# Kernel optimization log

Measured on AMD Instinct MI355X. Metric: run time of the kernel, lower is better.

## Reference

```python
import jax, jax.numpy as jnp
import numpy as np

T, B, I, H = 512, 64, 512, 1024


def setup_inputs() -> dict:
    key = jax.random.key(0)
    ks = jax.random.split(key, 7)
    s = 0.03  # keep recurrent dynamics stable
    return {
        "X": jax.random.normal(ks[0], (T, B, I), jnp.float32),
        "h0": jax.random.normal(ks[1], (B, H), jnp.float32) * 0.1,
        "c0": jax.random.normal(ks[2], (B, H), jnp.float32) * 0.1,
        "Wi": jax.random.normal(ks[3], (4, I, H), jnp.float32) * s,
        "Wh": jax.random.normal(ks[4], (4, H, H), jnp.float32) * s,
        "bi": jnp.zeros((4, H), jnp.float32),
        "bh": jnp.zeros((4, H), jnp.float32),
    }


def reference(X, h0, c0, Wi, Wh, bi, bh):
    # Gate order along axis 0 of Wi/Wh/bi/bh: f, i, g, o (matches the torch module's
    # linear_if/hf, linear_ii/hi, linear_ig/hg, linear_io/ho pairs).
    b = bi + bh  # [4, H] combined bias, mathematically identical

    def step(carry, x_t):
        h, c = carry
        # z: [4, B, H] = x @ Wi_g + h @ Wh_g + b_g for each gate g
        z = (jnp.einsum('bi,gih->gbh', x_t, Wi)
             + jnp.einsum('bh,ghk->gbk', h, Wh)
             + b[:, None, :])
        f = jax.nn.sigmoid(z[0])
        i = jax.nn.sigmoid(z[1])
        g = jnp.tanh(z[2])
        o = jax.nn.sigmoid(z[3])
        c_new = f * c + i * g
        h_new = o * jnp.tanh(c_new)
        return (h_new, c_new), h_new

    (h_n, c_n), outputs = jax.lax.scan(step, (h0, c0), X)
    return outputs, h_n, c_n
```

## Files before the change

kernel.cpp:

```cpp
#include <hip/hip_runtime.h>
#include <stdint.h>

#define T_STEPS 512
#define NB 64
#define NI 512
#define NH 1024
#define NBLK 128
#define DEPTH 32

typedef __attribute__((ext_vector_type(8))) short short8;
typedef __attribute__((ext_vector_type(4))) float floatx4;
typedef __attribute__((ext_vector_type(16))) float floatx16;
typedef __attribute__((ext_vector_type(4))) unsigned short ushortx4;

__device__ __forceinline__ unsigned short f2bf(float f) {
  union { float f; uint32_t u; } v; v.f = f;
  return (unsigned short)((v.u + 0x7FFFu + ((v.u >> 16) & 1u)) >> 16);
}
__device__ __forceinline__ float bf2f(unsigned short s) {
  union { uint32_t u; float f; } v; v.u = ((uint32_t)s) << 16; return v.f;
}
__device__ __forceinline__ float sigmoid_f(float x) {
  return 1.0f / (1.0f + __expf(-x));
}
__device__ __forceinline__ float tanh_f(float x) {
  float xx = fminf(fmaxf(x, -15.0f), 15.0f);
  float e = __expf(2.0f * xx);
  return (e - 1.0f) / (e + 1.0f);
}


__global__ void convert_x(const float* __restrict__ X, unsigned short* __restrict__ Xb) {
  int i = blockIdx.x * 256 + threadIdx.x;
  floatx4 x = ((const floatx4*)X)[i];
  ushortx4 o;
  o[0] = f2bf(x[0]); o[1] = f2bf(x[1]); o[2] = f2bf(x[2]); o[3] = f2bf(x[3]);
  ((ushortx4*)Xb)[i] = o;
}

__global__ void transpose_bf16(const float* __restrict__ in, unsigned short* __restrict__ outp,
                               int K, int N) {
  __shared__ float tile[64][65];
  int g = blockIdx.z;
  int k0 = blockIdx.x * 64, n0 = blockIdx.y * 64;
  int tx = threadIdx.x & 63, ty = threadIdx.x >> 6;
  const float* src = in + (size_t)g * K * N;
  unsigned short* dst = outp + (size_t)g * K * N;
#pragma unroll
  for (int i = 0; i < 16; i++) {
    int r = ty * 16 + i;
    tile[r][tx] = src[(size_t)(k0 + r) * N + n0 + tx];
  }
  __syncthreads();
#pragma unroll
  for (int i = 0; i < 16; i++) {
    int r = ty * 16 + i;
    dst[(size_t)(n0 + r) * K + k0 + tx] = f2bf(tile[tx][r]);
  }
}

__global__ void prep_small(const float* __restrict__ bi, const float* __restrict__ bh,
                           const float* __restrict__ h0, float* __restrict__ bias,
                           unsigned short* __restrict__ hbuf0, unsigned* __restrict__ flags) {
  int i = blockIdx.x * 256 + threadIdx.x;
  if (i < NBLK) flags[i] = 0u;
  if (i < 4 * NH) bias[i] = bi[i] + bh[i];
  if (i < NB * NH) hbuf0[i] = f2bf(h0[i]);
}

__global__ __launch_bounds__(256) void gemm_zx(
    const unsigned short* __restrict__ Xb,
    const unsigned short* __restrict__ WibT,
    const float* __restrict__ bias,
    unsigned short* __restrict__ Zq) {
  __shared__ __align__(16) unsigned short As[128][40];
  __shared__ __align__(16) unsigned short Bs[128][40];
  __shared__ __align__(16) unsigned short stg[16384];
  const int g = blockIdx.z;
  const int m0 = blockIdx.x * 128;
  const int n0 = blockIdx.y * 128;
  const int tid = threadIdx.x;
  const int lane = tid & 63;
  const int wave = tid >> 6;
  const int wm = wave & 1, wn = wave >> 1;
  const int fr = lane & 15;
  const int fq = (lane >> 4) * 8;

  const unsigned short* Bsrc = WibT + (size_t)g * NH * NI;

  floatx4 acc[4][4];
#pragma unroll
  for (int a = 0; a < 4; a++)
#pragma unroll
    for (int b = 0; b < 4; b++)
#pragma unroll
      for (int z = 0; z < 4; z++) acc[a][b][z] = 0.0f;

  for (int k0 = 0; k0 < NI; k0 += 32) {
#pragma unroll
    for (int it = 0; it < 2; it++) {
      int c = tid + it * 256;
      int row = c >> 2, kc = (c & 3) * 8;
      *(uint4*)(&As[row][kc]) = *(const uint4*)(Xb + (size_t)(m0 + row) * NI + k0 + kc);
      *(uint4*)(&Bs[row][kc]) = *(const uint4*)(Bsrc + (size_t)(n0 + row) * NI + k0 + kc);
    }
    __syncthreads();
    short8 af[4], bf[4];
#pragma unroll
    for (int ms = 0; ms < 4; ms++) af[ms] = *(const short8*)(&As[wm * 64 + ms * 16 + fr][fq]);
#pragma unroll
    for (int ns = 0; ns < 4; ns++) bf[ns] = *(const short8*)(&Bs[wn * 64 + ns * 16 + fr][fq]);
#pragma unroll
    for (int ms = 0; ms < 4; ms++)
#pragma unroll
      for (int ns = 0; ns < 4; ns++)
        acc[ms][ns] = __builtin_amdgcn_mfma_f32_16x16x32_bf16(af[ms], bf[ns], acc[ms][ns], 0, 0, 0);
    __syncthreads();
  }

#pragma unroll
  for (int ns = 0; ns < 4; ns++) {
    int jrel = wn * 64 + ns * 16 + fr;
    float bs = bias[g * NH + n0 + jrel];
    int bkp = jrel >> 3, jj = jrel & 7;
#pragma unroll
    for (int ms = 0; ms < 4; ms++) {
#pragma unroll
      for (int r = 0; r < 4; r++) {
        int mrel = wm * 64 + ms * 16 + (lane >> 4) * 4 + r;
        int tp = mrel >> 6, b = mrel & 63;
        int wm2 = b >> 5, row32 = b & 31;
        int half2 = (row32 >> 2) & 1;
        int rr = (row32 & 3) | ((row32 >> 3) << 2);
        int idx = (((((tp * 16 + bkp) * 2 + wm2) * 2 + half2) * 8 + jj) * 16) + rr;
        stg[idx] = f2bf(acc[ms][ns][r] + bs);
      }
    }
  }
  __syncthreads();
  const size_t t0 = (size_t)(m0 >> 6);
  const int bk0 = n0 >> 3;
#pragma unroll
  for (int tp = 0; tp < 2; tp++) {
    size_t gbase = (((t0 + tp) * 4 + g) * 128 + bk0) * 512;
#pragma unroll
    for (int c = 0; c < 4; c++) {
      int e = c * 2048 + tid * 8;
      *(uint4*)(Zq + gbase + e) = *(const uint4*)(stg + tp * 8192 + e);
    }
  }
}


template<int C>
__device__ __forceinline__ void load_a_c(const unsigned short* ap, short8 (&areg)[64]) {
  asm volatile("global_load_dwordx4 %0, %1, off offset:%2 sc0 sc1"
               : "=v"(areg[C]) : "v"(ap), "i"(C * 32));
}

template<int C>
__device__ __forceinline__ void load_b_c(const unsigned short* bfr, int lane, short8 (&bs)[64]) {
  bs[C] = *(const short8*)(&bfr[((size_t)(C * 64) + lane) * 8]);
}

template<int S, int I>
struct PrologR {
  static __device__ __forceinline__ void run(const unsigned short* ap, short8 (&areg)[64]) {
    load_a_c<(S + I) & 63>(ap, areg);
    PrologR<S, I + 1>::run(ap, areg);
  }
};
template<int S>
struct PrologR<S, DEPTH> {
  static __device__ __forceinline__ void run(const unsigned short*, short8 (&)[64]) {}
};

template<int S, int I>
struct ChunksR {
  static __device__ __forceinline__ void run(const unsigned short* ap, const unsigned short* bfr,
                                             int lane, short8 (&areg)[64], short8 (&bs)[64],
                                             floatx16& acc0, floatx16& acc1) {
    if constexpr (I + DEPTH < 64) load_a_c<(S + I + DEPTH) & 63>(ap, areg);
    if constexpr (I + 4 < 64) load_b_c<(S + I + 4) & 63>(bfr, lane, bs);
    constexpr int NOUT = (I + DEPTH < 64) ? DEPTH : (63 - I);
    constexpr int C = (S + I) & 63;
    asm volatile("s_waitcnt vmcnt(%1)" : "+v"(areg[C]) : "i"(NOUT) : "memory");
    if constexpr ((I & 1) == 0)
      acc0 = __builtin_amdgcn_mfma_f32_32x32x16_bf16(areg[C], bs[C], acc0, 0, 0, 0);
    else
      acc1 = __builtin_amdgcn_mfma_f32_32x32x16_bf16(areg[C], bs[C], acc1, 0, 0, 0);
    ChunksR<S, I + 1>::run(ap, bfr, lane, areg, bs, acc0, acc1);
  }
};
template<int S>
struct ChunksR<S, 64> {
  static __device__ __forceinline__ void run(const unsigned short*, const unsigned short*,
                                             int, short8 (&)[64], short8 (&)[64],
                                             floatx16&, floatx16&) {}
};

template<int S>
__device__ __forceinline__ void lstm_step(
    int t, const unsigned short* __restrict__ Zq, unsigned short* __restrict__ hbuf,
    unsigned* __restrict__ flags, float* __restrict__ out,
    const unsigned short* bfr, const unsigned long long* fpq,
    int tid, int lane, int wm, int nl, int g0, int jj, int half, int bk, int j0,
    size_t zoff, const int (&brow)[16], float (&creg)[16],
    uint4 (&zc)[2], uint4 (&zn)[2]) {
  const int hsz = NB * NH;

  if (t) {
    unsigned tgt = (unsigned)t;
    for (;;) {
      unsigned long long fv = __hip_atomic_load(fpq, __ATOMIC_RELAXED,
                                                __HIP_MEMORY_SCOPE_AGENT);
      unsigned a = (unsigned)fv, b2 = (unsigned)(fv >> 32);
      if (__all((int)((a >= tgt) && (b2 >= tgt)))) break;
      __builtin_amdgcn_s_sleep(1);
    }
  }
  asm volatile("s_waitcnt vmcnt(0)" ::: "memory");
  __builtin_amdgcn_sched_barrier(0);

  const unsigned short* hin = hbuf + (size_t)(t & 1) * hsz;
  unsigned short* hout = hbuf + (size_t)((t + 1) & 1) * hsz;
  const unsigned short* ap = hin + (size_t)(wm * 32 + nl) * NH + half * 8;

  floatx16 acc0, acc1;
#pragma unroll
  for (int z = 0; z < 16; z++) { acc0[z] = 0.0f; acc1[z] = 0.0f; }

  short8 areg[64];
  short8 bs[64];
  PrologR<S, 0>::run(ap, areg);
  load_b_c<(S + 0) & 63>(bfr, lane, bs);
  load_b_c<(S + 1) & 63>(bfr, lane, bs);
  load_b_c<(S + 2) & 63>(bfr, lane, bs);
  load_b_c<(S + 3) & 63>(bfr, lane, bs);
  ChunksR<S, 0>::run(ap, bfr, lane, areg, bs, acc0, acc1);
  __builtin_amdgcn_sched_barrier(0);

#pragma unroll
  for (int z = 0; z < 16; z++) acc0[z] += acc1[z];

  unsigned zd[8];
  zd[0] = zc[0].x; zd[1] = zc[0].y; zd[2] = zc[0].z; zd[3] = zc[0].w;
  zd[4] = zc[1].x; zd[5] = zc[1].y; zd[6] = zc[1].z; zd[7] = zc[1].w;

  float harr[16];
#pragma unroll
  for (int r = 0; r < 16; r++) {
    unsigned dw = zd[r >> 1];
    float zxv = bf2f((unsigned short)((r & 1) ? (dw >> 16) : (dw & 0xffffu)));
    float z0 = acc0[r] + zxv;
    float z1 = __shfl_xor(z0, 8);
    float z2 = __shfl_xor(z0, 16);
    float z3 = __shfl_xor(z1, 16);
    bool bb0 = (g0 & 1) != 0, bb1 = (g0 & 2) != 0;
    float zf = bb1 ? (bb0 ? z3 : z2) : (bb0 ? z1 : z0);
    float zi = bb1 ? (bb0 ? z2 : z3) : (bb0 ? z0 : z1);
    float zg = bb1 ? (bb0 ? z1 : z0) : (bb0 ? z3 : z2);
    float zo = bb1 ? (bb0 ? z0 : z1) : (bb0 ? z2 : z3);
    float fg = sigmoid_f(zf);
    float ig = sigmoid_f(zi);
    float gg = tanh_f(zg);
    float og = sigmoid_f(zo);
    float c = fg * creg[r] + ig * gg;
    creg[r] = c;
    float h = og * tanh_f(c);
    harr[r] = h;
    if (g0 == 0) {
      __hip_atomic_store(&hout[(size_t)brow[r] * NH + j0 + jj], f2bf(h),
                         __ATOMIC_RELAXED, __HIP_MEMORY_SCOPE_AGENT);
    }
  }

  if (t + 1 < T_STEPS) {
    asm volatile("s_waitcnt vmcnt(0)" ::: "memory");
    __syncthreads();
    if (tid == 0)
      __hip_atomic_store(flags + bk, (unsigned)(t + 1),
                         __ATOMIC_RELAXED, __HIP_MEMORY_SCOPE_AGENT);
    const unsigned short* zp = Zq + (size_t)(t + 1) * 262144 + zoff;
    asm volatile("global_load_dwordx4 %0, %1, off nt" : "=v"(zn[0]) : "v"(zp));
    asm volatile("global_load_dwordx4 %0, %1, off offset:16 nt" : "=v"(zn[1]) : "v"(zp));
  }

  if (g0 == 0) {
#pragma unroll
    for (int r = 0; r < 16; r++) {
      size_t oidx = (size_t)brow[r] * NH + j0 + jj;
      __builtin_nontemporal_store(harr[r], &out[(size_t)t * hsz + oidx]);
      if (t == T_STEPS - 1)
        __builtin_nontemporal_store(harr[r], &out[(size_t)T_STEPS * hsz + oidx]);
    }
  }
}

template<int S>
__device__ __forceinline__ void lstm_loop(
    const unsigned short* __restrict__ Zq, unsigned short* __restrict__ hbuf,
    unsigned* __restrict__ flags, float* __restrict__ out,
    const unsigned short* bfr, const unsigned long long* fpq,
    int tid, int lane, int wm, int nl, int g0, int jj, int half, int bk, int j0,
    size_t zoff, const int (&brow)[16], float (&creg)[16]) {
  uint4 zA[2], zB[2];
  {
    const unsigned short* zp = Zq + zoff;
    asm volatile("global_load_dwordx4 %0, %1, off nt" : "=v"(zA[0]) : "v"(zp));
    asm volatile("global_load_dwordx4 %0, %1, off offset:16 nt" : "=v"(zA[1]) : "v"(zp));
  }
  for (int t2 = 0; t2 < T_STEPS; t2 += 2) {
    lstm_step<S>(t2,     Zq, hbuf, flags, out, bfr, fpq, tid, lane, wm, nl, g0, jj,
                 half, bk, j0, zoff, brow, creg, zA, zB);
    lstm_step<S>(t2 + 1, Zq, hbuf, flags, out, bfr, fpq, tid, lane, wm, nl, g0, jj,
                 half, bk, j0, zoff, brow, creg, zB, zA);
  }
}

__global__ __launch_bounds__(128, 1) void lstm_persist(
    const unsigned short* __restrict__ Zq,
    const unsigned short* __restrict__ WhT,
    const float* __restrict__ c0,
    unsigned short* __restrict__ hbuf,
    unsigned* __restrict__ flags,
    float* __restrict__ out) {
  __shared__ __align__(16) unsigned short bfr[64 * 64 * 8];

  const int bk = blockIdx.x;
  const int j0 = bk * 8;
  const int tid = threadIdx.x;
  const int lane = tid & 63;
  const int wm = tid >> 6;
  const int nl = lane & 31;
  const int g0 = nl >> 3;
  const int jj = nl & 7;
  const int half = lane >> 5;

  for (int i = 0; i < 32; i++) {
    int f = tid + i * 128;
    int fl = f & 63, kk = f >> 6;
    int n = fl & 31;
    size_t wrow = (size_t)((n >> 3) * NH + j0 + (n & 7));
    int kb = kk * 16 + (fl >> 5) * 8;
    uint4 v = *(const uint4*)(WhT + wrow * NH + kb);
    *(uint4*)(&bfr[(size_t)f * 8]) = v;
  }

  float creg[16];
  int brow[16];
#pragma unroll
  for (int r = 0; r < 16; r++) {
    brow[r] = wm * 32 + (r & 3) + 8 * (r >> 2) + 4 * half;
    creg[r] = c0[(size_t)brow[r] * NH + j0 + jj];
  }
  __syncthreads();

  const unsigned long long* fpq = (const unsigned long long*)flags + lane;
  const size_t zoff = (((((size_t)g0 * 128 + bk) * 2 + wm) * 2 + half) * 8 + jj) * 16;

  switch (bk & 3) {
    case 0: lstm_loop<0>(Zq, hbuf, flags, out, bfr, fpq, tid, lane, wm, nl, g0, jj,
                         half, bk, j0, zoff, brow, creg); break;
    case 1: lstm_loop<16>(Zq, hbuf, flags, out, bfr, fpq, tid, lane, wm, nl, g0, jj,
                          half, bk, j0, zoff, brow, creg); break;
    case 2: lstm_loop<32>(Zq, hbuf, flags, out, bfr, fpq, tid, lane, wm, nl, g0, jj,
                          half, bk, j0, zoff, brow, creg); break;
    default: lstm_loop<48>(Zq, hbuf, flags, out, bfr, fpq, tid, lane, wm, nl, g0, jj,
                           half, bk, j0, zoff, brow, creg); break;
  }

  if (g0 == 0) {
#pragma unroll
    for (int r = 0; r < 16; r++)
      __builtin_nontemporal_store(
          creg[r], &out[(size_t)T_STEPS * NB * NH + NB * NH + (size_t)brow[r] * NH + j0 + jj]);
  }
}

extern "C" void kernel_launch(void* const* d_in, const int* in_sizes, int n_in,
                              void* d_out, int out_size, void* d_ws, size_t ws_size,
                              hipStream_t stream) {
  const float* X  = (const float*)d_in[0];
  const float* h0 = (const float*)d_in[1];
  const float* c0 = (const float*)d_in[2];
  const float* Wi = (const float*)d_in[3];
  const float* Wh = (const float*)d_in[4];
  const float* bi = (const float*)d_in[5];
  const float* bh = (const float*)d_in[6];
  float* out = (float*)d_out;

  uint8_t* ws = (uint8_t*)d_ws;
  size_t off = 0;
  auto alloc = [&](size_t bytes) -> void* {
    void* p = ws + off;
    off += (bytes + 255) & ~(size_t)255;
    return p;
  };
  unsigned short* Zq   = (unsigned short*)alloc((size_t)T_STEPS * NB * 4096 * 2);
  unsigned short* Xb   = (unsigned short*)alloc((size_t)T_STEPS * NB * NI * 2);
  unsigned short* WibT = (unsigned short*)alloc((size_t)4 * NH * NI * 2);
  unsigned short* WhT  = (unsigned short*)alloc((size_t)4 * NH * NH * 2);
  float* bias          = (float*)alloc((size_t)4 * NH * 4);
  unsigned short* hbuf = (unsigned short*)alloc((size_t)2 * NB * NH * 2);
  unsigned* flags      = (unsigned*)alloc((size_t)NBLK * 32 * 4);

  if (off > ws_size) {
    hipMemsetAsync(d_out, 0x7F, (size_t)out_size * 4, stream);
    return;
  }

  convert_x<<<16384, 256, 0, stream>>>(X, Xb);
  transpose_bf16<<<dim3(8, 16, 4), 256, 0, stream>>>(Wi, WibT, NI, NH);
  transpose_bf16<<<dim3(16, 16, 4), 256, 0, stream>>>(Wh, WhT, NH, NH);
  prep_small<<<256, 256, 0, stream>>>(bi, bh, h0, bias, hbuf, flags);
  gemm_zx<<<dim3(256, 8, 4), 256, 0, stream>>>(Xb, WibT, bias, Zq);

  lstm_persist<<<dim3(NBLK), dim3(128), 0, stream>>>(Zq, WhT, c0, hbuf, flags, out);
}
```

Measured before the change: 5.881 ms.

## Use per-XCD leader blocks to poll global flags and relay readiness locally

Each persistent block now takes a rank within its XCD from an atomic counter. Only the first block per XCD polls all 128 global step flags. That leader then invalidates its caches and publishes the step to a per-XCD flag, which the other blocks on that XCD poll. The h loads drop the sc0 sc1 cache-bypass bits and rely on explicit buffer_inv instead, so h reads can hit the L2. This is meant to cut cross-XCD flag polling traffic and h-load latency, at the cost of an extra relay hop per step and correctness that depends on the invalidates and on the flag region being sized correctly.

```diff
diff --git a/kernel.cpp b/kernel.cpp
--- a/kernel.cpp
+++ b/kernel.cpp
@@ -63,7 +63,7 @@
                            const float* __restrict__ h0, float* __restrict__ bias,
                            unsigned short* __restrict__ hbuf0, unsigned* __restrict__ flags) {
   int i = blockIdx.x * 256 + threadIdx.x;
-  if (i < NBLK) flags[i] = 0u;
+  if (i < NBLK * 32) flags[i] = 0u;
   if (i < 4 * NH) bias[i] = bi[i] + bh[i];
   if (i < NB * NH) hbuf0[i] = f2bf(h0[i]);
 }
@@ -154,7 +154,7 @@
 
 template<int C>
 __device__ __forceinline__ void load_a_c(const unsigned short* ap, short8 (&areg)[64]) {
-  asm volatile("global_load_dwordx4 %0, %1, off offset:%2 sc0 sc1"
+  asm volatile("global_load_dwordx4 %0, %1, off offset:%2"
                : "=v"(areg[C]) : "v"(ap), "i"(C * 32));
 }
 
@@ -204,6 +204,7 @@
     int t, const unsigned short* __restrict__ Zq, unsigned short* __restrict__ hbuf,
     unsigned* __restrict__ flags, float* __restrict__ out,
     const unsigned short* bfr, const unsigned long long* fpq,
+    unsigned* xcdf, bool leader,
     int tid, int lane, int wm, int nl, int g0, int jj, int half, int bk, int j0,
     size_t zoff, const int (&brow)[16], float (&creg)[16],
     uint4 (&zc)[2], uint4 (&zn)[2]) {
@@ -211,12 +212,23 @@
 
   if (t) {
     unsigned tgt = (unsigned)t;
-    for (;;) {
-      unsigned long long fv = __hip_atomic_load(fpq, __ATOMIC_RELAXED,
-                                                __HIP_MEMORY_SCOPE_AGENT);
-      unsigned a = (unsigned)fv, b2 = (unsigned)(fv >> 32);
-      if (__all((int)((a >= tgt) && (b2 >= tgt)))) break;
-      __builtin_amdgcn_s_sleep(1);
+    if (leader) {
+      for (;;) {
+        unsigned long long fv = __hip_atomic_load(fpq, __ATOMIC_RELAXED,
+                                                  __HIP_MEMORY_SCOPE_AGENT);
+        unsigned a = (unsigned)fv, b2 = (unsigned)(fv >> 32);
+        if (__all((int)((a >= tgt) && (b2 >= tgt)))) break;
+        __builtin_amdgcn_s_sleep(1);
+      }
+      asm volatile("buffer_inv sc0 sc1" ::: "memory");
+      asm volatile("s_waitcnt vmcnt(0)" ::: "memory");
+      __syncthreads();
+      if (tid == 0)
+        __hip_atomic_store(xcdf, tgt, __ATOMIC_RELAXED, __HIP_MEMORY_SCOPE_AGENT);
+    } else {
+      asm volatile("buffer_inv sc0" ::: "memory");
+      while (__hip_atomic_load(xcdf, __ATOMIC_RELAXED, __HIP_MEMORY_SCOPE_AGENT) < tgt)
+        __builtin_amdgcn_s_sleep(1);
     }
   }
   asm volatile("s_waitcnt vmcnt(0)" ::: "memory");
@@ -302,6 +314,7 @@
     const unsigned short* __restrict__ Zq, unsigned short* __restrict__ hbuf,
     unsigned* __restrict__ flags, float* __restrict__ out,
     const unsigned short* bfr, const unsigned long long* fpq,
+    unsigned* xcdf, bool leader,
     int tid, int lane, int wm, int nl, int g0, int jj, int half, int bk, int j0,
     size_t zoff, const int (&brow)[16], float (&creg)[16]) {
   uint4 zA[2], zB[2];
@@ -311,10 +324,10 @@
     asm volatile("global_load_dwordx4 %0, %1, off offset:16 nt" : "=v"(zA[1]) : "v"(zp));
   }
   for (int t2 = 0; t2 < T_STEPS; t2 += 2) {
-    lstm_step<S>(t2,     Zq, hbuf, flags, out, bfr, fpq, tid, lane, wm, nl, g0, jj,
-                 half, bk, j0, zoff, brow, creg, zA, zB);
-    lstm_step<S>(t2 + 1, Zq, hbuf, flags, out, bfr, fpq, tid, lane, wm, nl, g0, jj,
-                 half, bk, j0, zoff, brow, creg, zB, zA);
+    lstm_step<S>(t2,     Zq, hbuf, flags, out, bfr, fpq, xcdf, leader, tid, lane, wm,
+                 nl, g0, jj, half, bk, j0, zoff, brow, creg, zA, zB);
+    lstm_step<S>(t2 + 1, Zq, hbuf, flags, out, bfr, fpq, xcdf, leader, tid, lane, wm,
+                 nl, g0, jj, half, bk, j0, zoff, brow, creg, zB, zA);
   }
 }
 
@@ -326,6 +339,7 @@
     unsigned* __restrict__ flags,
     float* __restrict__ out) {
   __shared__ __align__(16) unsigned short bfr[64 * 64 * 8];
+  __shared__ int s_rank;
 
   const int bk = blockIdx.x;
   const int j0 = bk * 8;
@@ -337,6 +351,11 @@
   const int jj = nl & 7;
   const int half = lane >> 5;
 
+  unsigned xcd;
+  asm("s_getreg_b32 %0, hwreg(HW_REG_XCC_ID)" : "=s"(xcd));
+  xcd &= 7u;
+  if (tid == 0) s_rank = (int)atomicAdd(&flags[1024 + xcd], 1u);
+
   for (int i = 0; i < 32; i++) {
     int f = tid + i * 128;
     int fl = f & 63, kk = f >> 6;
@@ -355,19 +374,21 @@
     creg[r] = c0[(size_t)brow[r] * NH + j0 + jj];
   }
   __syncthreads();
+  const bool leader = (s_rank == 0);
 
   const unsigned long long* fpq = (const unsigned long long*)flags + lane;
+  unsigned* xcdf = flags + 2048 + (size_t)xcd * 32;
   const size_t zoff = (((((size_t)g0 * 128 + bk) * 2 + wm) * 2 + half) * 8 + jj) * 16;
 
   switch (bk & 3) {
-    case 0: lstm_loop<0>(Zq, hbuf, flags, out, bfr, fpq, tid, lane, wm, nl, g0, jj,
-                         half, bk, j0, zoff, brow, creg); break;
-    case 1: lstm_loop<16>(Zq, hbuf, flags, out, bfr, fpq, tid, lane, wm, nl, g0, jj,
-                          half, bk, j0, zoff, brow, creg); break;
-    case 2: lstm_loop<32>(Zq, hbuf, flags, out, bfr, fpq, tid, lane, wm, nl, g0, jj,
-                          half, bk, j0, zoff, brow, creg); break;
-    default: lstm_loop<48>(Zq, hbuf, flags, out, bfr, fpq, tid, lane, wm, nl, g0, jj,
-                           half, bk, j0, zoff, brow, creg); break;
+    case 0: lstm_loop<0>(Zq, hbuf, flags, out, bfr, fpq, xcdf, leader, tid, lane, wm,
+                         nl, g0, jj, half, bk, j0, zoff, brow, creg); break;
+    case 1: lstm_loop<16>(Zq, hbuf, flags, out, bfr, fpq, xcdf, leader, tid, lane, wm,
+                          nl, g0, jj, half, bk, j0, zoff, brow, creg); break;
+    case 2: lstm_loop<32>(Zq, hbuf, flags, out, bfr, fpq, xcdf, leader, tid, lane, wm,
+                          nl, g0, jj, half, bk, j0, zoff, brow, creg); break;
+    default: lstm_loop<48>(Zq, hbuf, flags, out, bfr, fpq, xcdf, leader, tid, lane, wm,
+                           nl, g0, jj, half, bk, j0, zoff, brow, creg); break;
   }
 
   if (g0 == 0) {
```

Measured after the change: 6.080 ms. 1.03x slower.

## Halve persistent LSTM blocks to 64, each with four waves covering sixteen hidden columns

Applied to the files above, without the earlier changes.

The persistent recurrent kernel now uses 64 blocks of 256 threads instead of 128 blocks of 128, so each block owns 16 hidden columns split across two wave-column groups. The Zx layout from the input GEMM, the LDS weight layout, the gate-lane mapping (gates now sit in adjacent lanes, shuffled by xor 1/2) and the flag polling (one 32-bit flag per lane, 64 lanes matching 64 blocks) are all rearranged to match. The aim is to halve the number of blocks taking part in each per-step grid synchronisation and to cut flag traffic, at the cost of fewer CUs doing the recurrent GEMM and twice the LDS weight footprint per block. Output stores also switch from nontemporal to regular stores.

```diff
diff --git a/kernel.cpp b/kernel.cpp
--- a/kernel.cpp
+++ b/kernel.cpp
@@ -5,7 +5,7 @@
 #define NB 64
 #define NI 512
 #define NH 1024
-#define NBLK 128
+#define NBLK 64
 #define DEPTH 32
 
 typedef __attribute__((ext_vector_type(8))) short short8;
@@ -63,7 +63,7 @@
                            const float* __restrict__ h0, float* __restrict__ bias,
                            unsigned short* __restrict__ hbuf0, unsigned* __restrict__ flags) {
   int i = blockIdx.x * 256 + threadIdx.x;
-  if (i < NBLK) flags[i] = 0u;
+  if (i < 4096) flags[i] = 0u;
   if (i < 4 * NH) bias[i] = bi[i] + bh[i];
   if (i < NB * NH) hbuf0[i] = f2bf(h0[i]);
 }
@@ -82,7 +82,7 @@
   const int tid = threadIdx.x;
   const int lane = tid & 63;
   const int wave = tid >> 6;
-  const int wm = wave & 1, wn = wave >> 1;
+  const int wmg = wave & 1, wng = wave >> 1;
   const int fr = lane & 15;
   const int fq = (lane >> 4) * 8;
 
@@ -107,9 +107,9 @@
     __syncthreads();
     short8 af[4], bf[4];
 #pragma unroll
-    for (int ms = 0; ms < 4; ms++) af[ms] = *(const short8*)(&As[wm * 64 + ms * 16 + fr][fq]);
-#pragma unroll
-    for (int ns = 0; ns < 4; ns++) bf[ns] = *(const short8*)(&Bs[wn * 64 + ns * 16 + fr][fq]);
+    for (int ms = 0; ms < 4; ms++) af[ms] = *(const short8*)(&As[wmg * 64 + ms * 16 + fr][fq]);
+#pragma unroll
+    for (int ns = 0; ns < 4; ns++) bf[ns] = *(const short8*)(&Bs[wng * 64 + ns * 16 + fr][fq]);
 #pragma unroll
     for (int ms = 0; ms < 4; ms++)
 #pragma unroll
@@ -120,29 +120,30 @@
 
 #pragma unroll
   for (int ns = 0; ns < 4; ns++) {
-    int jrel = wn * 64 + ns * 16 + fr;
+    int jrel = wng * 64 + ns * 16 + fr;
     float bs = bias[g * NH + n0 + jrel];
-    int bkp = jrel >> 3, jj = jrel & 7;
+    int q_rel = jrel >> 4, wn = (jrel >> 3) & 1, jjr = jrel & 7;
 #pragma unroll
     for (int ms = 0; ms < 4; ms++) {
 #pragma unroll
       for (int r = 0; r < 4; r++) {
-        int mrel = wm * 64 + ms * 16 + (lane >> 4) * 4 + r;
+        int mrel = wmg * 64 + ms * 16 + (lane >> 4) * 4 + r;
         int tp = mrel >> 6, b = mrel & 63;
         int wm2 = b >> 5, row32 = b & 31;
         int half2 = (row32 >> 2) & 1;
         int rr = (row32 & 3) | ((row32 >> 3) << 2);
-        int idx = (((((tp * 16 + bkp) * 2 + wm2) * 2 + half2) * 8 + jj) * 16) + rr;
+        int idx = tp * 8192 + q_rel * 1024 +
+                  (((wn * 2 + wm2) * 2 + half2) * 8 + jjr) * 16 + rr;
         stg[idx] = f2bf(acc[ms][ns][r] + bs);
       }
     }
   }
   __syncthreads();
   const size_t t0 = (size_t)(m0 >> 6);
-  const int bk0 = n0 >> 3;
+  const int q0 = n0 >> 4;
 #pragma unroll
   for (int tp = 0; tp < 2; tp++) {
-    size_t gbase = (((t0 + tp) * 4 + g) * 128 + bk0) * 512;
+    size_t gbase = ((((t0 + tp) * 4 + g) * 64) + q0) * 1024;
 #pragma unroll
     for (int c = 0; c < 4; c++) {
       int e = c * 2048 + tid * 8;
@@ -159,8 +160,8 @@
 }
 
 template<int C>
-__device__ __forceinline__ void load_b_c(const unsigned short* bfr, int lane, short8 (&bs)[64]) {
-  bs[C] = *(const short8*)(&bfr[((size_t)(C * 64) + lane) * 8]);
+__device__ __forceinline__ void load_b_c(const unsigned short* bq, short8 (&bs)[64]) {
+  bs[C] = *(const short8*)(bq + (size_t)C * 1024);
 }
 
 template<int S, int I>
@@ -177,11 +178,11 @@
 
 template<int S, int I>
 struct ChunksR {
-  static __device__ __forceinline__ void run(const unsigned short* ap, const unsigned short* bfr,
-                                             int lane, short8 (&areg)[64], short8 (&bs)[64],
+  static __device__ __forceinline__ void run(const unsigned short* ap, const unsigned short* bq,
+                                             short8 (&areg)[64], short8 (&bs)[64],
                                              floatx16& acc0, floatx16& acc1) {
     if constexpr (I + DEPTH < 64) load_a_c<(S + I + DEPTH) & 63>(ap, areg);
-    if constexpr (I + 4 < 64) load_b_c<(S + I + 4) & 63>(bfr, lane, bs);
+    if constexpr (I + 4 < 64) load_b_c<(S + I + 4) & 63>(bq, bs);
     constexpr int NOUT = (I + DEPTH < 64) ? DEPTH : (63 - I);
     constexpr int C = (S + I) & 63;
     asm volatile("s_waitcnt vmcnt(%1)" : "+v"(areg[C]) : "i"(NOUT) : "memory");
@@ -189,13 +190,13 @@
       acc0 = __builtin_amdgcn_mfma_f32_32x32x16_bf16(areg[C], bs[C], acc0, 0, 0, 0);
     else
       acc1 = __builtin_amdgcn_mfma_f32_32x32x16_bf16(areg[C], bs[C], acc1, 0, 0, 0);
-    ChunksR<S, I + 1>::run(ap, bfr, lane, areg, bs, acc0, acc1);
+    ChunksR<S, I + 1>::run(ap, bq, areg, bs, acc0, acc1);
   }
 };
 template<int S>
 struct ChunksR<S, 64> {
   static __device__ __forceinline__ void run(const unsigned short*, const unsigned short*,
-                                             int, short8 (&)[64], short8 (&)[64],
+                                             short8 (&)[64], short8 (&)[64],
                                              floatx16&, floatx16&) {}
 };
 
@@ -203,21 +204,17 @@
 __device__ __forceinline__ void lstm_step(
     int t, const unsigned short* __restrict__ Zq, unsigned short* __restrict__ hbuf,
     unsigned* __restrict__ flags, float* __restrict__ out,
-    const unsigned short* bfr, const unsigned long long* fpq,
-    int tid, int lane, int wm, int nl, int g0, int jj, int half, int bk, int j0,
+    const unsigned short* bq, const unsigned* fp,
+    int tid, int lane, int wm, int nl, int g0, int jcol, int half, int bk,
     size_t zoff, const int (&brow)[16], float (&creg)[16],
     uint4 (&zc)[2], uint4 (&zn)[2]) {
   const int hsz = NB * NH;
 
   if (t) {
     unsigned tgt = (unsigned)t;
-    for (;;) {
-      unsigned long long fv = __hip_atomic_load(fpq, __ATOMIC_RELAXED,
-                                                __HIP_MEMORY_SCOPE_AGENT);
-      unsigned a = (unsigned)fv, b2 = (unsigned)(fv >> 32);
-      if (__all((int)((a >= tgt) && (b2 >= tgt)))) break;
+    while (!__all((int)(__hip_atomic_load(fp, __ATOMIC_RELAXED,
+                                          __HIP_MEMORY_SCOPE_AGENT) >= tgt)))
       __builtin_amdgcn_s_sleep(1);
-    }
   }
   asm volatile("s_waitcnt vmcnt(0)" ::: "memory");
   __builtin_amdgcn_sched_barrier(0);
@@ -233,11 +230,11 @@
   short8 areg[64];
   short8 bs[64];
   PrologR<S, 0>::run(ap, areg);
-  load_b_c<(S + 0) & 63>(bfr, lane, bs);
-  load_b_c<(S + 1) & 63>(bfr, lane, bs);
-  load_b_c<(S + 2) & 63>(bfr, lane, bs);
-  load_b_c<(S + 3) & 63>(bfr, lane, bs);
-  ChunksR<S, 0>::run(ap, bfr, lane, areg, bs, acc0, acc1);
+  load_b_c<(S + 0) & 63>(bq, bs);
+  load_b_c<(S + 1) & 63>(bq, bs);
+  load_b_c<(S + 2) & 63>(bq, bs);
+  load_b_c<(S + 3) & 63>(bq, bs);
+  ChunksR<S, 0>::run(ap, bq, areg, bs, acc0, acc1);
   __builtin_amdgcn_sched_barrier(0);
 
 #pragma unroll
@@ -253,9 +250,9 @@
     unsigned dw = zd[r >> 1];
     float zxv = bf2f((unsigned short)((r & 1) ? (dw >> 16) : (dw & 0xffffu)));
     float z0 = acc0[r] + zxv;
-    float z1 = __shfl_xor(z0, 8);
-    float z2 = __shfl_xor(z0, 16);
-    float z3 = __shfl_xor(z1, 16);
+    float z1 = __shfl_xor(z0, 1);
+    float z2 = __shfl_xor(z0, 2);
+    float z3 = __shfl_xor(z1, 2);
     bool bb0 = (g0 & 1) != 0, bb1 = (g0 & 2) != 0;
     float zf = bb1 ? (bb0 ? z3 : z2) : (bb0 ? z1 : z0);
     float zi = bb1 ? (bb0 ? z2 : z3) : (bb0 ? z0 : z1);
@@ -270,7 +267,7 @@
     float h = og * tanh_f(c);
     harr[r] = h;
     if (g0 == 0) {
-      __hip_atomic_store(&hout[(size_t)brow[r] * NH + j0 + jj], f2bf(h),
+      __hip_atomic_store(&hout[(size_t)brow[r] * NH + jcol], f2bf(h),
                          __ATOMIC_RELAXED, __HIP_MEMORY_SCOPE_AGENT);
     }
   }
@@ -289,10 +286,9 @@
   if (g0 == 0) {
 #pragma unroll
     for (int r = 0; r < 16; r++) {
-      size_t oidx = (size_t)brow[r] * NH + j0 + jj;
-      __builtin_nontemporal_store(harr[r], &out[(size_t)t * hsz + oidx]);
-      if (t == T_STEPS - 1)
-        __builtin_nontemporal_store(harr[r], &out[(size_t)T_STEPS * hsz + oidx]);
+      size_t oidx = (size_t)brow[r] * NH + jcol;
+      out[(size_t)t * hsz + oidx] = harr[r];
+      if (t == T_STEPS - 1) out[(size_t)T_STEPS * hsz + oidx] = harr[r];
     }
   }
 }
@@ -301,8 +297,8 @@
 __device__ __forceinline__ void lstm_loop(
     const unsigned short* __restrict__ Zq, unsigned short* __restrict__ hbuf,
     unsigned* __restrict__ flags, float* __restrict__ out,
-    const unsigned short* bfr, const unsigned long long* fpq,
-    int tid, int lane, int wm, int nl, int g0, int jj, int half, int bk, int j0,
+    const unsigned short* bq, const unsigned* fp,
+    int tid, int lane, int wm, int nl, int g0, int jcol, int half, int bk,
     size_t zoff, const int (&brow)[16], float (&creg)[16]) {
   uint4 zA[2], zB[2];
   {
@@ -311,39 +307,40 @@
     asm volatile("global_load_dwordx4 %0, %1, off offset:16 nt" : "=v"(zA[1]) : "v"(zp));
   }
   for (int t2 = 0; t2 < T_STEPS; t2 += 2) {
-    lstm_step<S>(t2,     Zq, hbuf, flags, out, bfr, fpq, tid, lane, wm, nl, g0, jj,
-                 half, bk, j0, zoff, brow, creg, zA, zB);
-    lstm_step<S>(t2 + 1, Zq, hbuf, flags, out, bfr, fpq, tid, lane, wm, nl, g0, jj,
-                 half, bk, j0, zoff, brow, creg, zB, zA);
-  }
-}
-
-__global__ __launch_bounds__(128, 1) void lstm_persist(
+    lstm_step<S>(t2,     Zq, hbuf, flags, out, bq, fp, tid, lane, wm, nl, g0, jcol,
+                 half, bk, zoff, brow, creg, zA, zB);
+    lstm_step<S>(t2 + 1, Zq, hbuf, flags, out, bq, fp, tid, lane, wm, nl, g0, jcol,
+                 half, bk, zoff, brow, creg, zB, zA);
+  }
+}
+
+__global__ __launch_bounds__(256, 1) void lstm_persist(
     const unsigned short* __restrict__ Zq,
     const unsigned short* __restrict__ WhT,
     const float* __restrict__ c0,
     unsigned short* __restrict__ hbuf,
     unsigned* __restrict__ flags,
     float* __restrict__ out) {
-  __shared__ __align__(16) unsigned short bfr[64 * 64 * 8];
+  __shared__ __align__(16) unsigned short bfr[64 * 64 * 2 * 8];
 
   const int bk = blockIdx.x;
-  const int j0 = bk * 8;
+  const int j0 = bk * 16;
   const int tid = threadIdx.x;
   const int lane = tid & 63;
-  const int wm = tid >> 6;
+  const int wave = tid >> 6;
+  const int wm = wave & 1;
+  const int wn = wave >> 1;
   const int nl = lane & 31;
-  const int g0 = nl >> 3;
-  const int jj = nl & 7;
+  const int g0 = nl & 3;
+  const int jjr = nl >> 2;
   const int half = lane >> 5;
+  const int jcol = j0 + wn * 8 + jjr;
 
   for (int i = 0; i < 32; i++) {
-    int f = tid + i * 128;
-    int fl = f & 63, kk = f >> 6;
-    int n = fl & 31;
-    size_t wrow = (size_t)((n >> 3) * NH + j0 + (n & 7));
-    int kb = kk * 16 + (fl >> 5) * 8;
-    uint4 v = *(const uint4*)(WhT + wrow * NH + kb);
+    int f = tid + i * 256;
+    int kk = f >> 7, c = (f >> 1) & 63, hf = f & 1;
+    size_t wrow = (size_t)(c & 3) * NH + j0 + (c >> 2);
+    uint4 v = *(const uint4*)(WhT + wrow * NH + kk * 16 + hf * 8);
     *(uint4*)(&bfr[(size_t)f * 8]) = v;
   }
 
@@ -352,29 +349,29 @@
 #pragma unroll
   for (int r = 0; r < 16; r++) {
     brow[r] = wm * 32 + (r & 3) + 8 * (r >> 2) + 4 * half;
-    creg[r] = c0[(size_t)brow[r] * NH + j0 + jj];
+    creg[r] = c0[(size_t)brow[r] * NH + jcol];
   }
   __syncthreads();
 
-  const unsigned long long* fpq = (const unsigned long long*)flags + lane;
-  const size_t zoff = (((((size_t)g0 * 128 + bk) * 2 + wm) * 2 + half) * 8 + jj) * 16;
+  const unsigned* fp = flags + lane;
+  const unsigned short* bq = bfr + ((size_t)(wn * 32 + nl) * 2 + half) * 8;
+  const size_t zoff = ((((((size_t)g0 * 64 + bk) * 2 + wn) * 2 + wm) * 2 + half) * 8 + jjr) * 16;
 
   switch (bk & 3) {
-    case 0: lstm_loop<0>(Zq, hbuf, flags, out, bfr, fpq, tid, lane, wm, nl, g0, jj,
-                         half, bk, j0, zoff, brow, creg); break;
-    case 1: lstm_loop<16>(Zq, hbuf, flags, out, bfr, fpq, tid, lane, wm, nl, g0, jj,
-                          half, bk, j0, zoff, brow, creg); break;
-    case 2: lstm_loop<32>(Zq, hbuf, flags, out, bfr, fpq, tid, lane, wm, nl, g0, jj,
-                          half, bk, j0, zoff, brow, creg); break;
-    default: lstm_loop<48>(Zq, hbuf, flags, out, bfr, fpq, tid, lane, wm, nl, g0, jj,
-                           half, bk, j0, zoff, brow, creg); break;
+    case 0: lstm_loop<0>(Zq, hbuf, flags, out, bq, fp, tid, lane, wm, nl, g0, jcol,
+                         half, bk, zoff, brow, creg); break;
+    case 1: lstm_loop<16>(Zq, hbuf, flags, out, bq, fp, tid, lane, wm, nl, g0, jcol,
+                          half, bk, zoff, brow, creg); break;
+    case 2: lstm_loop<32>(Zq, hbuf, flags, out, bq, fp, tid, lane, wm, nl, g0, jcol,
+                          half, bk, zoff, brow, creg); break;
+    default: lstm_loop<48>(Zq, hbuf, flags, out, bq, fp, tid, lane, wm, nl, g0, jcol,
+                           half, bk, zoff, brow, creg); break;
   }
 
   if (g0 == 0) {
 #pragma unroll
     for (int r = 0; r < 16; r++)
-      __builtin_nontemporal_store(
-          creg[r], &out[(size_t)T_STEPS * NB * NH + NB * NH + (size_t)brow[r] * NH + j0 + jj]);
+      out[(size_t)T_STEPS * NB * NH + NB * NH + (size_t)brow[r] * NH + jcol] = creg[r];
   }
 }
 
@@ -403,7 +400,7 @@
   unsigned short* WhT  = (unsigned short*)alloc((size_t)4 * NH * NH * 2);
   float* bias          = (float*)alloc((size_t)4 * NH * 4);
   unsigned short* hbuf = (unsigned short*)alloc((size_t)2 * NB * NH * 2);
-  unsigned* flags      = (unsigned*)alloc((size_t)NBLK * 32 * 4);
+  unsigned* flags      = (unsigned*)alloc((size_t)4096 * 4);
 
   if (off > ws_size) {
     hipMemsetAsync(d_out, 0x7F, (size_t)out_size * 4, stream);
@@ -416,5 +413,5 @@
   prep_small<<<256, 256, 0, stream>>>(bi, bh, h0, bias, hbuf, flags);
   gemm_zx<<<dim3(256, 8, 4), 256, 0, stream>>>(Xb, WibT, bias, Zq);
 
-  lstm_persist<<<dim3(NBLK), dim3(128), 0, stream>>>(Zq, WhT, c0, hbuf, flags, out);
-}
+  lstm_persist<<<dim3(NBLK), dim3(256), 0, stream>>>(Zq, WhT, c0, hbuf, flags, out);
+}
```

Result: slower. 7.277 ms (+23.7%).

## Replace flag-based inter-block barrier with sentinel-valued h buffers and triple buffering

Applied to the files above, without the earlier changes.

Drops the per-step flag polling and __syncthreads/flag publish. Each block now reads the h chunk directly and spins until no 0xFFFF sentinel remains, using three rotating h buffers so the one two steps ahead can be cleared while the next is written. This is meant to remove the barrier round trip, letting consumers start on data as soon as it lands. The cost is extra reloads and a possible false stall if a genuine bf16 value equals 0xFFFF (a NaN pattern), plus subtle memory-ordering risk.

```diff
diff --git a/kernel.cpp b/kernel.cpp
--- a/kernel.cpp
+++ b/kernel.cpp
@@ -61,11 +61,11 @@
 
 __global__ void prep_small(const float* __restrict__ bi, const float* __restrict__ bh,
                            const float* __restrict__ h0, float* __restrict__ bias,
-                           unsigned short* __restrict__ hbuf0, unsigned* __restrict__ flags) {
+                           unsigned short* __restrict__ hbuf) {
   int i = blockIdx.x * 256 + threadIdx.x;
-  if (i < NBLK) flags[i] = 0u;
   if (i < 4 * NH) bias[i] = bi[i] + bh[i];
-  if (i < NB * NH) hbuf0[i] = f2bf(h0[i]);
+  if (i < NB * NH) hbuf[i] = f2bf(h0[i]);
+  if (i < NB * NH) ((unsigned*)hbuf)[NB * NH / 2 + i] = 0xFFFFFFFFu;
 }
 
 __global__ __launch_bounds__(256) void gemm_zx(
@@ -152,6 +152,15 @@
 }
 
 
+__device__ __forceinline__ bool chunk_stale(const short8& a) {
+  union { short8 s; unsigned u[4]; } x; x.s = a;
+  unsigned m0, m1;
+  asm("v_pk_max_u16 %0, %1, %2" : "=v"(m0) : "v"(x.u[0]), "v"(x.u[1]));
+  asm("v_pk_max_u16 %0, %1, %2" : "=v"(m1) : "v"(x.u[2]), "v"(x.u[3]));
+  asm("v_pk_max_u16 %0, %0, %1" : "+v"(m0) : "v"(m1));
+  return ((m0 & 0xFFFFu) == 0xFFFFu) || ((m0 >> 16) == 0xFFFFu);
+}
+
 template<int C>
 __device__ __forceinline__ void load_a_c(const unsigned short* ap, short8 (&areg)[64]) {
   asm volatile("global_load_dwordx4 %0, %1, off offset:%2 sc0 sc1"
@@ -185,6 +194,13 @@
     constexpr int NOUT = (I + DEPTH < 64) ? DEPTH : (63 - I);
     constexpr int C = (S + I) & 63;
     asm volatile("s_waitcnt vmcnt(%1)" : "+v"(areg[C]) : "i"(NOUT) : "memory");
+    bool st = chunk_stale(areg[C]);
+    while (__any((int)st)) {
+      asm volatile("global_load_dwordx4 %0, %1, off offset:%2 sc0 sc1"
+                   : "=v"(areg[C]) : "v"(ap), "i"(C * 32));
+      asm volatile("s_waitcnt vmcnt(0)" : "+v"(areg[C]) :: "memory");
+      st = chunk_stale(areg[C]);
+    }
     if constexpr ((I & 1) == 0)
       acc0 = __builtin_amdgcn_mfma_f32_32x32x16_bf16(areg[C], bs[C], acc0, 0, 0, 0);
     else
@@ -202,28 +218,18 @@
 template<int S>
 __device__ __forceinline__ void lstm_step(
     int t, const unsigned short* __restrict__ Zq, unsigned short* __restrict__ hbuf,
-    unsigned* __restrict__ flags, float* __restrict__ out,
-    const unsigned short* bfr, const unsigned long long* fpq,
+    float* __restrict__ out, const unsigned short* bfr,
     int tid, int lane, int wm, int nl, int g0, int jj, int half, int bk, int j0,
     size_t zoff, const int (&brow)[16], float (&creg)[16],
     uint4 (&zc)[2], uint4 (&zn)[2]) {
   const int hsz = NB * NH;
 
-  if (t) {
-    unsigned tgt = (unsigned)t;
-    for (;;) {
-      unsigned long long fv = __hip_atomic_load(fpq, __ATOMIC_RELAXED,
-                                                __HIP_MEMORY_SCOPE_AGENT);
-      unsigned a = (unsigned)fv, b2 = (unsigned)(fv >> 32);
-      if (__all((int)((a >= tgt) && (b2 >= tgt)))) break;
-      __builtin_amdgcn_s_sleep(1);
-    }
-  }
   asm volatile("s_waitcnt vmcnt(0)" ::: "memory");
   __builtin_amdgcn_sched_barrier(0);
 
-  const unsigned short* hin = hbuf + (size_t)(t & 1) * hsz;
-  unsigned short* hout = hbuf + (size_t)((t + 1) & 1) * hsz;
+  const unsigned short* hin = hbuf + (size_t)(t % 3) * hsz;
+  unsigned short* hout = hbuf + (size_t)((t + 1) % 3) * hsz;
+  unsigned* hclr = (unsigned*)(hbuf + (size_t)((t + 2) % 3) * hsz);
   const unsigned short* ap = hin + (size_t)(wm * 32 + nl) * NH + half * 8;
 
   floatx16 acc0, acc1;
@@ -240,6 +246,16 @@
   ChunksR<S, 0>::run(ap, bfr, lane, areg, bs, acc0, acc1);
   __builtin_amdgcn_sched_barrier(0);
 
+  if (t + 1 < T_STEPS) {
+#pragma unroll
+    for (int u = 0; u < 2; u++) {
+      int e = tid * 2 + u;
+      int r = e >> 2, d = e & 3;
+      __hip_atomic_store(hclr + (size_t)r * (NH / 2) + (j0 >> 1) + d, 0xFFFFFFFFu,
+                         __ATOMIC_RELAXED, __HIP_MEMORY_SCOPE_AGENT);
+    }
+  }
+
 #pragma unroll
   for (int z = 0; z < 16; z++) acc0[z] += acc1[z];
 
@@ -248,6 +264,7 @@
   zd[4] = zc[1].x; zd[5] = zc[1].y; zd[6] = zc[1].z; zd[7] = zc[1].w;
 
   float harr[16];
+  unsigned short hus[16];
 #pragma unroll
   for (int r = 0; r < 16; r++) {
     unsigned dw = zd[r >> 1];
@@ -269,21 +286,15 @@
     creg[r] = c;
     float h = og * tanh_f(c);
     harr[r] = h;
-    if (g0 == 0) {
-      __hip_atomic_store(&hout[(size_t)brow[r] * NH + j0 + jj], f2bf(h),
+    hus[r] = f2bf(h);
+  }
+
+  asm volatile("s_waitcnt vmcnt(0)" ::: "memory");
+  if (t + 1 < T_STEPS && g0 == 0) {
+#pragma unroll
+    for (int r = 0; r < 16; r++)
+      __hip_atomic_store(&hout[(size_t)brow[r] * NH + j0 + jj], hus[r],
                          __ATOMIC_RELAXED, __HIP_MEMORY_SCOPE_AGENT);
-    }
-  }
-
-  if (t + 1 < T_STEPS) {
-    asm volatile("s_waitcnt vmcnt(0)" ::: "memory");
-    __syncthreads();
-    if (tid == 0)
-      __hip_atomic_store(flags + bk, (unsigned)(t + 1),
-                         __ATOMIC_RELAXED, __HIP_MEMORY_SCOPE_AGENT);
-    const unsigned short* zp = Zq + (size_t)(t + 1) * 262144 + zoff;
-    asm volatile("global_load_dwordx4 %0, %1, off nt" : "=v"(zn[0]) : "v"(zp));
-    asm volatile("global_load_dwordx4 %0, %1, off offset:16 nt" : "=v"(zn[1]) : "v"(zp));
   }
 
   if (g0 == 0) {
@@ -295,13 +306,18 @@
         __builtin_nontemporal_store(harr[r], &out[(size_t)T_STEPS * hsz + oidx]);
     }
   }
+
+  if (t + 1 < T_STEPS) {
+    const unsigned short* zp = Zq + (size_t)(t + 1) * 262144 + zoff;
+    asm volatile("global_load_dwordx4 %0, %1, off nt" : "=v"(zn[0]) : "v"(zp));
+    asm volatile("global_load_dwordx4 %0, %1, off offset:16 nt" : "=v"(zn[1]) : "v"(zp));
+  }
 }
 
 template<int S>
 __device__ __forceinline__ void lstm_loop(
     const unsigned short* __restrict__ Zq, unsigned short* __restrict__ hbuf,
-    unsigned* __restrict__ flags, float* __restrict__ out,
-    const unsigned short* bfr, const unsigned long long* fpq,
+    float* __restrict__ out, const unsigned short* bfr,
     int tid, int lane, int wm, int nl, int g0, int jj, int half, int bk, int j0,
     size_t zoff, const int (&brow)[16], float (&creg)[16]) {
   uint4 zA[2], zB[2];
@@ -311,10 +327,10 @@
     asm volatile("global_load_dwordx4 %0, %1, off offset:16 nt" : "=v"(zA[1]) : "v"(zp));
   }
   for (int t2 = 0; t2 < T_STEPS; t2 += 2) {
-    lstm_step<S>(t2,     Zq, hbuf, flags, out, bfr, fpq, tid, lane, wm, nl, g0, jj,
-                 half, bk, j0, zoff, brow, creg, zA, zB);
-    lstm_step<S>(t2 + 1, Zq, hbuf, flags, out, bfr, fpq, tid, lane, wm, nl, g0, jj,
-                 half, bk, j0, zoff, brow, creg, zB, zA);
+    lstm_step<S>(t2,     Zq, hbuf, out, bfr, tid, lane, wm, nl, g0, jj, half,
+                 bk, j0, zoff, brow, creg, zA, zB);
+    lstm_step<S>(t2 + 1, Zq, hbuf, out, bfr, tid, lane, wm, nl, g0, jj, half,
+                 bk, j0, zoff, brow, creg, zB, zA);
   }
 }
 
@@ -323,7 +339,6 @@
     const unsigned short* __restrict__ WhT,
     const float* __restrict__ c0,
     unsigned short* __restrict__ hbuf,
-    unsigned* __restrict__ flags,
     float* __restrict__ out) {
   __shared__ __align__(16) unsigned short bfr[64 * 64 * 8];
 
@@ -356,18 +371,17 @@
   }
   __syncthreads();
 
-  const unsigned long long* fpq = (const unsigned long long*)flags + lane;
   const size_t zoff = (((((size_t)g0 * 128 + bk) * 2 + wm) * 2 + half) * 8 + jj) * 16;
 
   switch (bk & 3) {
-    case 0: lstm_loop<0>(Zq, hbuf, flags, out, bfr, fpq, tid, lane, wm, nl, g0, jj,
-                         half, bk, j0, zoff, brow, creg); break;
-    case 1: lstm_loop<16>(Zq, hbuf, flags, out, bfr, fpq, tid, lane, wm, nl, g0, jj,
-                          half, bk, j0, zoff, brow, creg); break;
-    case 2: lstm_loop<32>(Zq, hbuf, flags, out, bfr, fpq, tid, lane, wm, nl, g0, jj,
-                          half, bk, j0, zoff, brow, creg); break;
-    default: lstm_loop<48>(Zq, hbuf, flags, out, bfr, fpq, tid, lane, wm, nl, g0, jj,
-                           half, bk, j0, zoff, brow, creg); break;
+    case 0: lstm_loop<0>(Zq, hbuf, out, bfr, tid, lane, wm, nl, g0, jj, half,
+                         bk, j0, zoff, brow, creg); break;
+    case 1: lstm_loop<16>(Zq, hbuf, out, bfr, tid, lane, wm, nl, g0, jj, half,
+                          bk, j0, zoff, brow, creg); break;
+    case 2: lstm_loop<32>(Zq, hbuf, out, bfr, tid, lane, wm, nl, g0, jj, half,
+                          bk, j0, zoff, brow, creg); break;
+    default: lstm_loop<48>(Zq, hbuf, out, bfr, tid, lane, wm, nl, g0, jj, half,
+                           bk, j0, zoff, brow, creg); break;
   }
 
   if (g0 == 0) {
@@ -402,8 +416,7 @@
   unsigned short* WibT = (unsigned short*)alloc((size_t)4 * NH * NI * 2);
   unsigned short* WhT  = (unsigned short*)alloc((size_t)4 * NH * NH * 2);
   float* bias          = (float*)alloc((size_t)4 * NH * 4);
-  unsigned short* hbuf = (unsigned short*)alloc((size_t)2 * NB * NH * 2);
-  unsigned* flags      = (unsigned*)alloc((size_t)NBLK * 32 * 4);
+  unsigned short* hbuf = (unsigned short*)alloc((size_t)3 * NB * NH * 2);
 
   if (off > ws_size) {
     hipMemsetAsync(d_out, 0x7F, (size_t)out_size * 4, stream);
@@ -413,8 +426,8 @@
   convert_x<<<16384, 256, 0, stream>>>(X, Xb);
   transpose_bf16<<<dim3(8, 16, 4), 256, 0, stream>>>(Wi, WibT, NI, NH);
   transpose_bf16<<<dim3(16, 16, 4), 256, 0, stream>>>(Wh, WhT, NH, NH);
-  prep_small<<<256, 256, 0, stream>>>(bi, bh, h0, bias, hbuf, flags);
+  prep_small<<<256, 256, 0, stream>>>(bi, bh, h0, bias, hbuf);
   gemm_zx<<<dim3(256, 8, 4), 256, 0, stream>>>(Xb, WibT, bias, Zq);
 
-  lstm_persist<<<dim3(NBLK), dim3(128), 0, stream>>>(Zq, WhT, c0, hbuf, flags, out);
-}
+  lstm_persist<<<dim3(NBLK), dim3(128), 0, stream>>>(Zq, WhT, c0, hbuf, out);
+}
```

Result: slower. 8.796 ms (+49.6%).
